# Kernel tuning notes

Measured on AMD Instinct MI355X. Metric: run time of the kernel, lower is better.

Reference implementation:

```python
import jax, jax.numpy as jnp
import numpy as np

BN_EPS = 1e-5

def conv1x1(x, w, b):
    # x: [B,C,H,W], w: [O,C], b: [O] -> [B,O,H,W]
    return jnp.einsum('bchw,oc->bohw', x, w) + b[None, :, None, None]

def maxpool2x2(x):
    B, C, H, W = x.shape
    return x.reshape(B, C, H // 2, 2, W // 2, 2).max(axis=(3, 5))

def setup_inputs() -> dict:
    key = jax.random.key(0)
    ks = jax.random.split(key, 12)
    B, C, Ci, H, W = 8, 256, 128, 64, 64
    s_in = 1.0 / np.sqrt(C)
    s_mid = 1.0 / np.sqrt(Ci)
    return {
        'x': jax.random.normal(ks[0], (B, C, H, W), jnp.float32),
        'y': jax.random.normal(ks[1], (B, C, H, W), jnp.float32),
        'theta_w': jax.random.normal(ks[2], (Ci, C), jnp.float32) * s_in,
        'theta_b': jax.random.normal(ks[3], (Ci,), jnp.float32) * s_in,
        'phi_w': jax.random.normal(ks[4], (Ci, C), jnp.float32) * s_in,
        'phi_b': jax.random.normal(ks[5], (Ci,), jnp.float32) * s_in,
        'g_w': jax.random.normal(ks[6], (Ci, C), jnp.float32) * s_in,
        'g_b': jax.random.normal(ks[7], (Ci,), jnp.float32) * s_in,
        'w_w': jax.random.normal(ks[8], (C, Ci), jnp.float32) * s_mid,
        'w_b': jax.random.normal(ks[9], (C,), jnp.float32) * s_mid,
        'bn_gamma': jax.random.normal(ks[10], (C,), jnp.float32),
        'bn_beta': jax.random.normal(ks[11], (C,), jnp.float32),
    }

def reference(x, y, theta_w, theta_b, phi_w, phi_b, g_w, g_b, w_w, w_b, bn_gamma, bn_beta):
    B, C, H, W = x.shape
    Ci = theta_w.shape[0]
    # Q: [B, N, Ci] from x (no subsample)
    theta_x = conv1x1(x, theta_w, theta_b).reshape(B, Ci, H * W).transpose(0, 2, 1)
    # K: [B, Ci, M] and V: [B, M, Ci] from y (2x2 maxpool subsample)
    phi_x = maxpool2x2(conv1x1(y, phi_w, phi_b)).reshape(B, Ci, -1)
    g_x = maxpool2x2(conv1x1(y, g_w, g_b)).reshape(B, Ci, -1).transpose(0, 2, 1)
    # unscaled dot-product attention, softmax over keys
    f = jnp.einsum('bnc,bcm->bnm', theta_x, phi_x)        # [B, N, M]
    attn = jax.nn.softmax(f, axis=-1)
    out = jnp.einsum('bnm,bmc->bnc', attn, g_x)            # [B, N, Ci]
    out = out.transpose(0, 2, 1).reshape(B, Ci, H, W)
    # W projection (1x1 conv) + BatchNorm (batch statistics, training mode)
    wy = conv1x1(out, w_w, w_b)
    mean = wy.mean(axis=(0, 2, 3))
    var = wy.var(axis=(0, 2, 3))
    wy = (wy - mean[None, :, None, None]) * jax.lax.rsqrt(var[None, :, None, None] + BN_EPS)
    wy = wy * bn_gamma[None, :, None, None] + bn_beta[None, :, None, None]
    return wy + x
```

## Files before the change

kernel.cpp:

```cpp
#include <hip/hip_runtime.h>

#define B_  8
#define C_  256
#define CI_ 128
#define N_  4096
#define M_  1024

typedef unsigned short u16;
typedef _Float16 f16;
typedef __attribute__((ext_vector_type(8))) short short8;
typedef __attribute__((ext_vector_type(8))) _Float16 half8;
typedef __attribute__((ext_vector_type(4))) _Float16 half4;
typedef __attribute__((ext_vector_type(4))) float f32x4;

__device__ __forceinline__ u16 f2bf(float f) {
    unsigned int u = __float_as_uint(f);
    u += 0x7fffu + ((u >> 16) & 1u);
    return (u16)(u >> 16);
}
__device__ __forceinline__ float bf2f(u16 h) {
    return __uint_as_float(((unsigned int)h) << 16);
}

__global__ __launch_bounds__(256) void prep_w_kernel(
    const float* __restrict__ tw, const float* __restrict__ pw,
    const float* __restrict__ gw, const float* __restrict__ ww,
    f16* __restrict__ out_h)
{
    int t = blockIdx.x * 256 + threadIdx.x;
    int wsel = t >> 12, idx = t & 4095;
    int lane = idx & 63;
    const float* src; int F, Cdim;
    if (wsel == 3)      { src = ww; F = 16; Cdim = 128; }
    else if (wsel == 0) { src = tw; F = 8;  Cdim = 256; }
    else if (wsel == 1) { src = pw; F = 8;  Cdim = 256; }
    else                { src = gw; F = 8;  Cdim = 256; }
    int fk = idx >> 6;
    int ks = fk / F, f = fk - ks * F;
    int o = f * 16 + (lane & 15);
    int c = ks * 32 + (lane >> 4) * 8;
    const float* s = src + (size_t)o * Cdim + c;
    float4 v0 = *(const float4*)s;
    float4 v1 = *(const float4*)(s + 4);
    half8 hv;
    hv[0] = (f16)v0.x; hv[1] = (f16)v0.y; hv[2] = (f16)v0.z; hv[3] = (f16)v0.w;
    hv[4] = (f16)v1.x; hv[5] = (f16)v1.y; hv[6] = (f16)v1.z; hv[7] = (f16)v1.w;
    size_t oo = (size_t)wsel * 32768 + (size_t)idx * 8;
    *(half8*)&out_h[oo] = hv;
}

__global__ __launch_bounds__(256) void qconv_kernel(
    const float* __restrict__ x,
    const f16* __restrict__ Bfh, const float* __restrict__ bias,
    f16* __restrict__ qh_out)
{
    const int tid = threadIdx.x;
    const int wave = tid >> 6, lane = tid & 63;
    const int tx = lane & 15, quad = lane >> 4;
    const int id = blockIdx.x;
    const int ot = (id >> 3) & 1;
    const int p  = (id & 7) | ((id >> 4) << 3);
    const int nb = p & 63;
    const int b  = p >> 6;
    const int nw = nb * 64 + wave * 16;

    f32x4 acc[4];
    #pragma unroll
    for (int i = 0; i < 4; ++i) acc[i] = (f32x4){0.f, 0.f, 0.f, 0.f};

    #pragma unroll
    for (int ks = 0; ks < 8; ++ks) {
        const size_t cbase = ((size_t)b * C_ + ks * 32 + quad * 8) * N_ + nw + tx;
        float a[8];
        #pragma unroll
        for (int j = 0; j < 8; ++j) a[j] = x[cbase + (size_t)j * N_];
        half8 ah;
        #pragma unroll
        for (int j = 0; j < 8; ++j) ah[j] = (f16)a[j];
        #pragma unroll
        for (int fi = 0; fi < 4; ++fi) {
            int f = ot * 4 + fi;
            size_t bo = ((size_t)(ks * 8 + f) * 64 + lane) * 8;
            half8 bh = *(const half8*)&Bfh[bo];
            acc[fi] = __builtin_amdgcn_mfma_f32_16x16x32_f16(ah, bh, acc[fi], 0, 0, 0);
        }
    }

    #pragma unroll
    for (int fi = 0; fi < 4; ++fi) {
        int f = ot * 4 + fi;
        float bv = bias[f * 16 + tx];
        #pragma unroll
        for (int r = 0; r < 4; ++r) {
            size_t addr = ((size_t)(b * N_ + nw + quad * 4 + r)) * CI_ + f * 16 + tx;
            qh_out[addr] = (f16)(acc[fi][r] + bv);
        }
    }
}

__global__ __launch_bounds__(256) void kvconv_kernel(
    const float* __restrict__ y,
    const f16* __restrict__ PfH, const f16* __restrict__ GfH,
    const float* __restrict__ phib, const float* __restrict__ gb,
    f16* __restrict__ khi, u16* __restrict__ vf)
{
    const int tid = threadIdx.x;
    const int w = tid >> 6, lane = tid & 63;
    const int tx = lane & 15, quad = lane >> 4;
    const int id = blockIdx.x;
    const int ot = (id >> 3) & 1;
    const int p  = (id & 7) | ((id >> 4) << 3);
    const int t = p & 31;
    const int b = p >> 5;

    const size_t nA = (size_t)t * 128 + w * 16 + tx;
    const size_t nB = nA + 64;

    f32x4 accP[2][4], accG[2][4];
    #pragma unroll
    for (int i = 0; i < 2; ++i)
        #pragma unroll
        for (int j = 0; j < 4; ++j) {
            accP[i][j] = (f32x4){0.f, 0.f, 0.f, 0.f};
            accG[i][j] = (f32x4){0.f, 0.f, 0.f, 0.f};
        }

    #pragma unroll
    for (int ks = 0; ks < 8; ++ks) {
        const size_t cbase = ((size_t)b * C_ + ks * 32 + quad * 8) * N_;
        float a0[8], a1[8];
        #pragma unroll
        for (int j = 0; j < 8; ++j) {
            a0[j] = y[cbase + (size_t)j * N_ + nA];
            a1[j] = y[cbase + (size_t)j * N_ + nB];
        }
        half8 ah0, ah1;
        #pragma unroll
        for (int j = 0; j < 8; ++j) {
            ah0[j] = (f16)a0[j];
            ah1[j] = (f16)a1[j];
        }
        #pragma unroll
        for (int of = 0; of < 4; ++of) {
            int f = ot * 4 + of;
            size_t bo = ((size_t)(ks * 8 + f) * 64 + lane) * 8;
            half8 ph = *(const half8*)&PfH[bo];
            half8 gh = *(const half8*)&GfH[bo];
            accP[0][of] = __builtin_amdgcn_mfma_f32_16x16x32_f16(ah0, ph, accP[0][of], 0, 0, 0);
            accP[1][of] = __builtin_amdgcn_mfma_f32_16x16x32_f16(ah1, ph, accP[1][of], 0, 0, 0);
            accG[0][of] = __builtin_amdgcn_mfma_f32_16x16x32_f16(ah0, gh, accG[0][of], 0, 0, 0);
            accG[1][of] = __builtin_amdgcn_mfma_f32_16x16x32_f16(ah1, gh, accG[1][of], 0, 0, 0);
        }
    }

    #pragma unroll
    for (int of = 0; of < 4; ++of) {
        int ci = (ot * 4 + of) * 16 + tx;
        float pb = phib[ci], gbv = gb[ci];
        #pragma unroll
        for (int j = 0; j < 2; ++j) {
            float vP = fmaxf(fmaxf(accP[0][of][2 * j], accP[0][of][2 * j + 1]),
                             fmaxf(accP[1][of][2 * j], accP[1][of][2 * j + 1])) + pb;
            float vG = fmaxf(fmaxf(accG[0][of][2 * j], accG[0][of][2 * j + 1]),
                             fmaxf(accG[1][of][2 * j], accG[1][of][2 * j + 1])) + gbv;
            int mm = 8 * w + 2 * quad + j;
            int fragK = (mm >> 4) * 4 + (ci >> 5);
            int laneK = (((ci & 31) >> 3) << 4) + (mm & 15);
            size_t ka = (((size_t)(b * 32 + t) * 8 + fragK) * 64 + laneK) * 8 + (ci & 7);
            khi[ka] = (f16)vP;
            int fragV = ci >> 4;
            size_t va = (((size_t)(b * 32 + t) * 8 + fragV) * 64 + w * 16 + tx) * 8 + (2 * quad + j);
            vf[va] = f2bf(vG);
        }
    }
}

__global__ __launch_bounds__(256) void attn_kernel(
    const f16* __restrict__ Qh, const f16* __restrict__ Kf,
    const u16* __restrict__ Vf, f16* __restrict__ Oh)
{
    __shared__ __align__(16) f16 kh_sh[2][4096];
    __shared__ __align__(16) u16 vf_sh[2][4096];
    __shared__ __align__(16) u16 p_sh[4][16 * 40];

    const int tid = threadIdx.x;
    const int wave = tid >> 6, lane = tid & 63;
    const int tx = lane & 15, quad = lane >> 4;
    const int b = blockIdx.y;
    const int q0 = blockIdx.x * 64 + wave * 16;
    const float FM = 48.f;

    half8 qh[4];
    {
        const f16* qp = Qh + ((size_t)b * N_ + q0 + tx) * CI_ + quad * 8;
        #pragma unroll
        for (int ks = 0; ks < 4; ++ks) qh[ks] = *(const half8*)&qp[ks * 32];
    }

    f32x4 acc[8];
    #pragma unroll
    for (int f = 0; f < 8; ++f) acc[f] = (f32x4){0.f, 0.f, 0.f, 0.f};
    float lrun[4] = {0.f, 0.f, 0.f, 0.f};

    const f16* Khb = Kf + (size_t)b * 32 * 4096;
    const u16* Vb  = Vf + (size_t)b * 32 * 4096;

    half8 rk[2]; short8 rv[2];
    #pragma unroll
    for (int rp = 0; rp < 2; ++rp) {
        int idx = (tid + 256 * rp) * 8;
        rk[rp] = *(const half8*)&Khb[idx];
        rv[rp] = *(const short8*)&Vb[idx];
    }

    for (int ch = 0; ch < 32; ++ch) {
        const int cur = ch & 1;
        #pragma unroll
        for (int rp = 0; rp < 2; ++rp) {
            int idx = (tid + 256 * rp) * 8;
            *(half8*)&kh_sh[cur][idx] = rk[rp];
            *(short8*)&vf_sh[cur][idx] = rv[rp];
        }
        if (ch + 1 < 32) {
            #pragma unroll
            for (int rp = 0; rp < 2; ++rp) {
                int idx = (tid + 256 * rp) * 8;
                rk[rp] = *(const half8*)&Khb[(ch + 1) * 4096 + idx];
                rv[rp] = *(const short8*)&Vb[(ch + 1) * 4096 + idx];
            }
        }
        asm volatile("s_waitcnt lgkmcnt(0)" ::: "memory");
        __builtin_amdgcn_s_barrier();
        asm volatile("" ::: "memory");

        f32x4 s0 = (f32x4){0.f, 0.f, 0.f, 0.f};
        f32x4 s1 = (f32x4){0.f, 0.f, 0.f, 0.f};
        __builtin_amdgcn_s_setprio(1);
        #pragma unroll
        for (int ks = 0; ks < 4; ++ks) {
            half8 bh0 = *(const half8*)&kh_sh[cur][ks * 512 + lane * 8];
            half8 bh1 = *(const half8*)&kh_sh[cur][(4 + ks) * 512 + lane * 8];
            s0 = __builtin_amdgcn_mfma_f32_16x16x32_f16(qh[ks], bh0, s0, 0, 0, 0);
            s1 = __builtin_amdgcn_mfma_f32_16x16x32_f16(qh[ks], bh1, s1, 0, 0, 0);
        }
        __builtin_amdgcn_s_setprio(0);

        u16* pw_ = p_sh[wave];
        #pragma unroll
        for (int r = 0; r < 4; ++r) {
            float p0 = __expf(s0[r] - FM);
            float p1 = __expf(s1[r] - FM);
            lrun[r] += p0 + p1;
            pw_[(4 * quad + r) * 40 + tx]      = f2bf(p0);
            pw_[(4 * quad + r) * 40 + 16 + tx] = f2bf(p1);
        }
        asm volatile("s_waitcnt lgkmcnt(0)" ::: "memory");
        short8 pf = *(const short8*)&pw_[tx * 40 + quad * 8];

        __builtin_amdgcn_s_setprio(1);
        #pragma unroll
        for (int f = 0; f < 8; ++f) {
            short8 vb = *(const short8*)&vf_sh[cur][f * 512 + lane * 8];
            acc[f] = __builtin_amdgcn_mfma_f32_16x16x32_bf16(pf, vb, acc[f], 0, 0, 0);
        }
        __builtin_amdgcn_s_setprio(0);
    }

    #pragma unroll
    for (int d = 1; d < 16; d <<= 1) {
        #pragma unroll
        for (int r = 0; r < 4; ++r) lrun[r] += __shfl_xor(lrun[r], d);
    }
    float inv[4];
    #pragma unroll
    for (int r = 0; r < 4; ++r) inv[r] = 1.f / lrun[r];
    f16* Ob = Oh + ((size_t)b * N_ + q0) * CI_;
    #pragma unroll
    for (int f = 0; f < 8; ++f) {
        #pragma unroll
        for (int r = 0; r < 4; ++r)
            Ob[(size_t)(4 * quad + r) * CI_ + f * 16 + tx] = (f16)(acc[f][r] * inv[r]);
    }
}

__global__ __launch_bounds__(256) void wconv_mfma_kernel(
    const f16* __restrict__ Bh, const f16* __restrict__ Afh,
    const float* __restrict__ bias, f16* __restrict__ wy,
    float* __restrict__ part)
{
    const int tid = threadIdx.x;
    const int wave = tid >> 6, lane = tid & 63;
    const int tx = lane & 15, quad = lane >> 4;
    const int gnt = blockIdx.x;
    const int b = gnt >> 7;
    const int n0 = (gnt & 127) * 32;
    const int of0 = wave * 4;

    half8 wah[4][4];
    #pragma unroll
    for (int ks = 0; ks < 4; ++ks) {
        #pragma unroll
        for (int ff = 0; ff < 4; ++ff) {
            size_t aa = ((size_t)(ks * 16 + of0 + ff) * 64 + lane) * 8;
            wah[ks][ff] = *(const half8*)&Afh[aa];
        }
    }

    f32x4 acc[4][2];
    #pragma unroll
    for (int i = 0; i < 4; ++i)
        #pragma unroll
        for (int j = 0; j < 2; ++j) acc[i][j] = (f32x4){0.f, 0.f, 0.f, 0.f};

    #pragma unroll
    for (int ks = 0; ks < 4; ++ks) {
        half8 bh[2];
        #pragma unroll
        for (int nf = 0; nf < 2; ++nf) {
            size_t ba = ((size_t)(b * N_ + n0 + nf * 16 + tx)) * CI_ + ks * 32 + quad * 8;
            bh[nf] = *(const half8*)&Bh[ba];
        }
        #pragma unroll
        for (int ff = 0; ff < 4; ++ff)
            #pragma unroll
            for (int nf = 0; nf < 2; ++nf)
                acc[ff][nf] = __builtin_amdgcn_mfma_f32_16x16x32_f16(wah[ks][ff], bh[nf], acc[ff][nf], 0, 0, 0);
    }

    #pragma unroll
    for (int ff = 0; ff < 4; ++ff) {
        int fg = of0 + ff;
        #pragma unroll
        for (int r = 0; r < 4; ++r) {
            int o = fg * 16 + quad * 4 + r;
            float bo = bias[o];
            float ps = 0.f, pss = 0.f;
            #pragma unroll
            for (int nf = 0; nf < 2; ++nf) {
                float v = acc[ff][nf][r] + bo;
                wy[((size_t)b * C_ + o) * N_ + n0 + nf * 16 + tx] = (f16)v;
                ps += v; pss += v * v;
            }
            #pragma unroll
            for (int d = 1; d < 16; d <<= 1) {
                ps  += __shfl_xor(ps, d);
                pss += __shfl_xor(pss, d);
            }
            if (tx == 0) {
                part[(size_t)o * 1024 + gnt]          = ps;
                part[262144 + (size_t)o * 1024 + gnt] = pss;
            }
        }
    }
}

__global__ __launch_bounds__(256) void bn_reduce_kernel(
    const float* __restrict__ part, float* __restrict__ sums)
{
    int w = blockIdx.x * 4 + (threadIdx.x >> 6);
    int lane = threadIdx.x & 63;
    int p = w >> 8, o = w & 255;
    const float* src = part + (size_t)p * 262144 + (size_t)o * 1024;
    float s = 0.f;
    #pragma unroll
    for (int j = 0; j < 16; ++j) s += src[j * 64 + lane];
    #pragma unroll
    for (int d = 1; d < 64; d <<= 1) s += __shfl_xor(s, d);
    if (lane == 0) sums[p * 256 + o] = s;
}

__global__ __launch_bounds__(256) void bn_final_kernel(
    const f16* __restrict__ wy, const float* __restrict__ x,
    const float* __restrict__ gsum, const float* __restrict__ gsumsq,
    const float* __restrict__ gamma, const float* __restrict__ beta,
    float* __restrict__ out)
{
    int idx = blockIdx.x * 256 + threadIdx.x;
    size_t base = (size_t)idx * 4;
    int o = (int)((base >> 12) & 255);
    half4 wv = *(const half4*)&wy[base];
    float4 xv = *(const float4*)&x[base];
    const float invc = 1.f / 32768.f;
    float mean = gsum[o] * invc;
    float var  = gsumsq[o] * invc - mean * mean;
    float sc = gamma[o] * rsqrtf(var + 1e-5f);
    float sh = beta[o] - mean * sc;
    float4 r;
    r.x = (float)wv[0] * sc + sh + xv.x;
    r.y = (float)wv[1] * sc + sh + xv.y;
    r.z = (float)wv[2] * sc + sh + xv.z;
    r.w = (float)wv[3] * sc + sh + xv.w;
    *(float4*)&out[base] = r;
}

extern "C" void kernel_launch(void* const* d_in, const int* in_sizes, int n_in,
                              void* d_out, int out_size, void* d_ws, size_t ws_size,
                              hipStream_t stream) {
    (void)in_sizes; (void)n_in; (void)out_size; (void)ws_size;
    const float* x       = (const float*)d_in[0];
    const float* y       = (const float*)d_in[1];
    const float* theta_w = (const float*)d_in[2];
    const float* theta_b = (const float*)d_in[3];
    const float* phi_w   = (const float*)d_in[4];
    const float* phi_b   = (const float*)d_in[5];
    const float* g_w     = (const float*)d_in[6];
    const float* g_b     = (const float*)d_in[7];
    const float* w_w     = (const float*)d_in[8];
    const float* w_b     = (const float*)d_in[9];
    const float* bn_g    = (const float*)d_in[10];
    const float* bn_b    = (const float*)d_in[11];
    float* out = (float*)d_out;

    float* ws = (float*)d_ws;
    f16*   Qh   = (f16*)(ws);
    f16*   Kf   = (f16*)(ws + 2097152);
    u16*   Vfp  = (u16*)(ws + 2621440);
    f16*   Oh   = (f16*)(ws + 7405568);
    f16*   WY   = (f16*)(ws + 9502720);
    float* PART = ws + 13697024;
    f16*   Wfh  = (f16*)(ws + 14221312);
    float* SUMS = ws + 14286848;

    prep_w_kernel<<<64, 256, 0, stream>>>(theta_w, phi_w, g_w, w_w, Wfh);

    qconv_kernel<<<1024, 256, 0, stream>>>(x, Wfh, theta_b, Qh);
    kvconv_kernel<<<512, 256, 0, stream>>>(
        y, Wfh + 32768, Wfh + 65536, phi_b, g_b, Kf, Vfp);

    attn_kernel<<<dim3(64, 8), 256, 0, stream>>>(Qh, Kf, Vfp, Oh);

    wconv_mfma_kernel<<<1024, 256, 0, stream>>>(Oh, Wfh + 98304, w_b, WY, PART);
    bn_reduce_kernel<<<128, 256, 0, stream>>>(PART, SUMS);
    bn_final_kernel<<<8192, 256, 0, stream>>>(WY, x, SUMS, SUMS + 256, bn_g, bn_b, out);
}
```

Baseline: 203.2 us.

## Software-pipeline attention QK and PV across chunks; fuse BN reduction via atomics

The attention kernel now uses a three-slot LDS ring and software-pipelines the work: in each iteration the QK^T MFMAs for the current key chunk are issued together with the PV MFMAs for the previous chunk, with all LDS fragments loaded up front. The goal is to hide the exp/softmax and LDS round-trip latency behind matrix work. Blocks are remapped to a 1D grid with batch as the fastest index, which changes how K/V are shared in L2 across concurrently running blocks. The BN partial-sum buffer and its reduce kernel are replaced by float atomicAdds into sums that prep_w_kernel zeroes, saving one launch at the cost of atomic contention and non-deterministic summation order.

```diff
diff --git a/kernel.cpp b/kernel.cpp
--- a/kernel.cpp
+++ b/kernel.cpp
@@ -18,16 +18,14 @@
     u += 0x7fffu + ((u >> 16) & 1u);
     return (u16)(u >> 16);
 }
-__device__ __forceinline__ float bf2f(u16 h) {
-    return __uint_as_float(((unsigned int)h) << 16);
-}
 
 __global__ __launch_bounds__(256) void prep_w_kernel(
     const float* __restrict__ tw, const float* __restrict__ pw,
     const float* __restrict__ gw, const float* __restrict__ ww,
-    f16* __restrict__ out_h)
+    f16* __restrict__ out_h, float* __restrict__ sums)
 {
     int t = blockIdx.x * 256 + threadIdx.x;
+    if (t < 512) sums[t] = 0.f;
     int wsel = t >> 12, idx = t & 4095;
     int lane = idx & 63;
     const float* src; int F, Cdim;
@@ -179,15 +177,16 @@
     const f16* __restrict__ Qh, const f16* __restrict__ Kf,
     const u16* __restrict__ Vf, f16* __restrict__ Oh)
 {
-    __shared__ __align__(16) f16 kh_sh[2][4096];
-    __shared__ __align__(16) u16 vf_sh[2][4096];
+    __shared__ __align__(16) f16 kh_sh[3][4096];
+    __shared__ __align__(16) u16 vf_sh[3][4096];
     __shared__ __align__(16) u16 p_sh[4][16 * 40];
 
     const int tid = threadIdx.x;
     const int wave = tid >> 6, lane = tid & 63;
     const int tx = lane & 15, quad = lane >> 4;
-    const int b = blockIdx.y;
-    const int q0 = blockIdx.x * 64 + wave * 16;
+    const int id = blockIdx.x;
+    const int b = id & 7;
+    const int q0 = (id >> 3) * 64 + wave * 16;
     const float FM = 48.f;
 
     half8 qh[4];
@@ -204,31 +203,20 @@
 
     const f16* Khb = Kf + (size_t)b * 32 * 4096;
     const u16* Vb  = Vf + (size_t)b * 32 * 4096;
+    const int i0 = tid * 8, i1 = (tid + 256) * 8;
+    u16* pw_ = p_sh[wave];
 
     half8 rk[2]; short8 rv[2];
-    #pragma unroll
-    for (int rp = 0; rp < 2; ++rp) {
-        int idx = (tid + 256 * rp) * 8;
-        rk[rp] = *(const half8*)&Khb[idx];
-        rv[rp] = *(const short8*)&Vb[idx];
-    }
-
-    for (int ch = 0; ch < 32; ++ch) {
-        const int cur = ch & 1;
-        #pragma unroll
-        for (int rp = 0; rp < 2; ++rp) {
-            int idx = (tid + 256 * rp) * 8;
-            *(half8*)&kh_sh[cur][idx] = rk[rp];
-            *(short8*)&vf_sh[cur][idx] = rv[rp];
-        }
-        if (ch + 1 < 32) {
-            #pragma unroll
-            for (int rp = 0; rp < 2; ++rp) {
-                int idx = (tid + 256 * rp) * 8;
-                rk[rp] = *(const half8*)&Khb[(ch + 1) * 4096 + idx];
-                rv[rp] = *(const short8*)&Vb[(ch + 1) * 4096 + idx];
-            }
-        }
+    rk[0] = *(const half8*)&Khb[i0]; rk[1] = *(const half8*)&Khb[i1];
+    rv[0] = *(const short8*)&Vb[i0]; rv[1] = *(const short8*)&Vb[i1];
+
+    short8 pf;
+
+    {
+        *(half8*)&kh_sh[0][i0] = rk[0]; *(half8*)&kh_sh[0][i1] = rk[1];
+        *(short8*)&vf_sh[0][i0] = rv[0]; *(short8*)&vf_sh[0][i1] = rv[1];
+        rk[0] = *(const half8*)&Khb[4096 + i0]; rk[1] = *(const half8*)&Khb[4096 + i1];
+        rv[0] = *(const short8*)&Vb[4096 + i0]; rv[1] = *(const short8*)&Vb[4096 + i1];
         asm volatile("s_waitcnt lgkmcnt(0)" ::: "memory");
         __builtin_amdgcn_s_barrier();
         asm volatile("" ::: "memory");
@@ -238,14 +226,12 @@
         __builtin_amdgcn_s_setprio(1);
         #pragma unroll
         for (int ks = 0; ks < 4; ++ks) {
-            half8 bh0 = *(const half8*)&kh_sh[cur][ks * 512 + lane * 8];
-            half8 bh1 = *(const half8*)&kh_sh[cur][(4 + ks) * 512 + lane * 8];
+            half8 bh0 = *(const half8*)&kh_sh[0][ks * 512 + lane * 8];
+            half8 bh1 = *(const half8*)&kh_sh[0][(4 + ks) * 512 + lane * 8];
             s0 = __builtin_amdgcn_mfma_f32_16x16x32_f16(qh[ks], bh0, s0, 0, 0, 0);
             s1 = __builtin_amdgcn_mfma_f32_16x16x32_f16(qh[ks], bh1, s1, 0, 0, 0);
         }
         __builtin_amdgcn_s_setprio(0);
-
-        u16* pw_ = p_sh[wave];
         #pragma unroll
         for (int r = 0; r < 4; ++r) {
             float p0 = __expf(s0[r] - FM);
@@ -255,15 +241,68 @@
             pw_[(4 * quad + r) * 40 + 16 + tx] = f2bf(p1);
         }
         asm volatile("s_waitcnt lgkmcnt(0)" ::: "memory");
-        short8 pf = *(const short8*)&pw_[tx * 40 + quad * 8];
-
+        pf = *(const short8*)&pw_[tx * 40 + quad * 8];
+    }
+
+    int sI = 1, pI = 0;
+    for (int ch = 1; ch < 32; ++ch) {
+        f16* kdst = kh_sh[sI]; u16* vdst = vf_sh[sI];
+        *(half8*)&kdst[i0] = rk[0]; *(half8*)&kdst[i1] = rk[1];
+        *(short8*)&vdst[i0] = rv[0]; *(short8*)&vdst[i1] = rv[1];
+        {
+            int nch = ch + 1 < 32 ? ch + 1 : 31;
+            const f16* kp = Khb + (size_t)nch * 4096;
+            const u16* vp = Vb + (size_t)nch * 4096;
+            rk[0] = *(const half8*)&kp[i0]; rk[1] = *(const half8*)&kp[i1];
+            rv[0] = *(const short8*)&vp[i0]; rv[1] = *(const short8*)&vp[i1];
+        }
+        asm volatile("s_waitcnt lgkmcnt(0)" ::: "memory");
+        __builtin_amdgcn_s_barrier();
+        asm volatile("" ::: "memory");
+
+        const f16* ksrc = kh_sh[sI];
+        const u16* vsrc = vf_sh[pI];
+        half8 bh[8];
+        #pragma unroll
+        for (int ks = 0; ks < 8; ++ks) bh[ks] = *(const half8*)&ksrc[ks * 512 + lane * 8];
+        short8 vb[8];
+        #pragma unroll
+        for (int f = 0; f < 8; ++f) vb[f] = *(const short8*)&vsrc[f * 512 + lane * 8];
+
+        f32x4 s0 = (f32x4){0.f, 0.f, 0.f, 0.f};
+        f32x4 s1 = (f32x4){0.f, 0.f, 0.f, 0.f};
         __builtin_amdgcn_s_setprio(1);
         #pragma unroll
+        for (int ks = 0; ks < 4; ++ks) {
+            s0 = __builtin_amdgcn_mfma_f32_16x16x32_f16(qh[ks], bh[ks], s0, 0, 0, 0);
+            s1 = __builtin_amdgcn_mfma_f32_16x16x32_f16(qh[ks], bh[4 + ks], s1, 0, 0, 0);
+        }
+        #pragma unroll
+        for (int f = 0; f < 8; ++f)
+            acc[f] = __builtin_amdgcn_mfma_f32_16x16x32_bf16(pf, vb[f], acc[f], 0, 0, 0);
+        __builtin_amdgcn_s_setprio(0);
+
+        #pragma unroll
+        for (int r = 0; r < 4; ++r) {
+            float p0 = __expf(s0[r] - FM);
+            float p1 = __expf(s1[r] - FM);
+            lrun[r] += p0 + p1;
+            pw_[(4 * quad + r) * 40 + tx]      = f2bf(p0);
+            pw_[(4 * quad + r) * 40 + 16 + tx] = f2bf(p1);
+        }
+        asm volatile("s_waitcnt lgkmcnt(0)" ::: "memory");
+        pf = *(const short8*)&pw_[tx * 40 + quad * 8];
+
+        pI = sI; sI = (sI == 2) ? 0 : sI + 1;
+    }
+
+    {
+        const u16* vsrc = vf_sh[pI];
+        #pragma unroll
         for (int f = 0; f < 8; ++f) {
-            short8 vb = *(const short8*)&vf_sh[cur][f * 512 + lane * 8];
+            short8 vb = *(const short8*)&vsrc[f * 512 + lane * 8];
             acc[f] = __builtin_amdgcn_mfma_f32_16x16x32_bf16(pf, vb, acc[f], 0, 0, 0);
         }
-        __builtin_amdgcn_s_setprio(0);
     }
 
     #pragma unroll
@@ -286,7 +325,7 @@
 __global__ __launch_bounds__(256) void wconv_mfma_kernel(
     const f16* __restrict__ Bh, const f16* __restrict__ Afh,
     const float* __restrict__ bias, f16* __restrict__ wy,
-    float* __restrict__ part)
+    float* __restrict__ sums)
 {
     const int tid = threadIdx.x;
     const int wave = tid >> 6, lane = tid & 63;
@@ -347,26 +386,11 @@
                 pss += __shfl_xor(pss, d);
             }
             if (tx == 0) {
-                part[(size_t)o * 1024 + gnt]          = ps;
-                part[262144 + (size_t)o * 1024 + gnt] = pss;
+                atomicAdd(&sums[o], ps);
+                atomicAdd(&sums[256 + o], pss);
             }
         }
     }
-}
-
-__global__ __launch_bounds__(256) void bn_reduce_kernel(
-    const float* __restrict__ part, float* __restrict__ sums)
-{
-    int w = blockIdx.x * 4 + (threadIdx.x >> 6);
-    int lane = threadIdx.x & 63;
-    int p = w >> 8, o = w & 255;
-    const float* src = part + (size_t)p * 262144 + (size_t)o * 1024;
-    float s = 0.f;
-    #pragma unroll
-    for (int j = 0; j < 16; ++j) s += src[j * 64 + lane];
-    #pragma unroll
-    for (int d = 1; d < 64; d <<= 1) s += __shfl_xor(s, d);
-    if (lane == 0) sums[p * 256 + o] = s;
 }
 
 __global__ __launch_bounds__(256) void bn_final_kernel(
@@ -417,19 +441,17 @@
     u16*   Vfp  = (u16*)(ws + 2621440);
     f16*   Oh   = (f16*)(ws + 7405568);
     f16*   WY   = (f16*)(ws + 9502720);
-    float* PART = ws + 13697024;
     f16*   Wfh  = (f16*)(ws + 14221312);
     float* SUMS = ws + 14286848;
 
-    prep_w_kernel<<<64, 256, 0, stream>>>(theta_w, phi_w, g_w, w_w, Wfh);
+    prep_w_kernel<<<64, 256, 0, stream>>>(theta_w, phi_w, g_w, w_w, Wfh, SUMS);
 
     qconv_kernel<<<1024, 256, 0, stream>>>(x, Wfh, theta_b, Qh);
     kvconv_kernel<<<512, 256, 0, stream>>>(
         y, Wfh + 32768, Wfh + 65536, phi_b, g_b, Kf, Vfp);
 
-    attn_kernel<<<dim3(64, 8), 256, 0, stream>>>(Qh, Kf, Vfp, Oh);
-
-    wconv_mfma_kernel<<<1024, 256, 0, stream>>>(Oh, Wfh + 98304, w_b, WY, PART);
-    bn_reduce_kernel<<<128, 256, 0, stream>>>(PART, SUMS);
+    attn_kernel<<<512, 256, 0, stream>>>(Qh, Kf, Vfp, Oh);
+
+    wconv_mfma_kernel<<<1024, 256, 0, stream>>>(Oh, Wfh + 98304, w_b, WY, SUMS);
     bn_final_kernel<<<8192, 256, 0, stream>>>(WY, x, SUMS, SUMS + 256, bn_g, bn_b, out);
 }
```

Measured after the change: 345.6 us. 1.7x slower.
